# Performance work log

Measured on AMD Instinct MI355X. Metric: run time of the kernel, lower is better.

Reference implementation:

```python
import jax, jax.numpy as jnp
import numpy as np

T, B, H, V = 128, 32, 1024, 32000


def setup_inputs() -> dict:
    key = jax.random.key(0)
    ks = jax.random.split(key, 8)
    scale = 1.0 / np.sqrt(H)
    return {
        "input": jax.random.normal(ks[0], (T, B, H), dtype=jnp.float32),
        "hidden": jnp.zeros((B, H), dtype=jnp.float32),
        "w_ic": jax.random.uniform(ks[1], (H, H), jnp.float32, -scale, scale),
        "w_ix": jax.random.uniform(ks[2], (H, H), jnp.float32, -scale, scale),
        "w_fc": jax.random.uniform(ks[3], (H, H), jnp.float32, -scale, scale),
        "w_fx": jax.random.uniform(ks[4], (H, H), jnp.float32, -scale, scale),
        "b_i": jnp.zeros((H,), dtype=jnp.float32),
        "b_f": jnp.zeros((H,), dtype=jnp.float32),
        "W_out": jax.random.uniform(ks[5], (V, H), jnp.float32, -scale, scale),
        "b_out": jnp.zeros((V,), dtype=jnp.float32),
    }


def reference(input, hidden, w_ic, w_ix, w_fc, w_fx, b_i, b_f, W_out, b_out):
    # Precompute input projections for all timesteps: [T, B, H]
    ix = jnp.einsum("tbh,kh->tbk", input, w_ix)
    fx = jnp.einsum("tbh,kh->tbk", input, w_fx)

    def step(c, xs):
        ix_t, fx_t, x_t = xs
        i_t = jax.nn.sigmoid(c @ w_ic.T + b_i + ix_t)
        f_t = jax.nn.sigmoid(c @ w_fc.T + b_f + fx_t)
        c_new = i_t * x_t + f_t * c  # RAN gated-additive update
        return c_new, c_new

    hidden_final, outputs = jax.lax.scan(step, hidden, (ix, fx, input))
    logits = jnp.einsum("tbh,vh->tbv", outputs, W_out) + b_out
    log_probs = jax.nn.log_softmax(logits, axis=-1)
    return log_probs, hidden_final
```

## Files before the change

kernel.cpp:

```cpp
#include <hip/hip_runtime.h>

typedef __attribute__((ext_vector_type(4))) float f32x4;
typedef __attribute__((ext_vector_type(8))) short bf16x8;

#define T_DIM 128
#define B_DIM 32
#define H_DIM 1024
#define V_DIM 32000
#define MROWS 4096
#define NBLK 64
#define CSTEP 32768
#define WSTRIDE 1028

__device__ __forceinline__ ushort f2bf(float f){
  union { float f; unsigned u; } x; x.f = f;
  unsigned u = x.u;
  unsigned r = (u + 0x7fffu + ((u >> 16) & 1u)) >> 16;
  return (ushort)r;
}
__device__ __forceinline__ float bf2f(ushort h){
  union { unsigned u; float f; } x; x.u = ((unsigned)h) << 16;
  return x.f;
}

__device__ __forceinline__ void async_copy16(void* lds, const void* g){
  __builtin_amdgcn_global_load_lds((const __attribute__((address_space(1))) void*)g,
                                   (__attribute__((address_space(3))) void*)lds, 16, 0, 0);
}

__global__ void cast_bf16_kernel(const float* __restrict__ s, ushort* __restrict__ d, int n4){
  int stride = gridDim.x * blockDim.x;
  for (int i = blockIdx.x*blockDim.x + threadIdx.x; i < n4; i += stride){
    float4 v = ((const float4*)s)[i];
    ushort4 o = make_ushort4(f2bf(v.x), f2bf(v.y), f2bf(v.z), f2bf(v.w));
    ((ushort4*)d)[i] = o;
  }
}

__global__ void cast_split_kernel(const float* __restrict__ s, ushort* __restrict__ dh,
                                  ushort* __restrict__ dl, int n4){
  int stride = gridDim.x * blockDim.x;
  for (int i = blockIdx.x*blockDim.x + threadIdx.x; i < n4; i += stride){
    float4 v = ((const float4*)s)[i];
    ushort4 h = make_ushort4(f2bf(v.x), f2bf(v.y), f2bf(v.z), f2bf(v.w));
    ushort4 l = make_ushort4(f2bf(v.x - bf2f(h.x)), f2bf(v.y - bf2f(h.y)),
                             f2bf(v.z - bf2f(h.z)), f2bf(v.w - bf2f(h.w)));
    ((ushort4*)dh)[i] = h;
    ((ushort4*)dl)[i] = l;
  }
}

__global__ __launch_bounds__(256) void gemm_bt(
    const ushort* __restrict__ A, const ushort* __restrict__ B,
    float* __restrict__ C, const float* __restrict__ bias,
    int N, int K, int NTN, int order, int achunk,
    float* __restrict__ pmax, float* __restrict__ psum)
{
  __shared__ ushort lA[128*32];
  __shared__ ushort lB[128*32];
  __shared__ float pmS[4][64], psS[4][64];
  int tid = threadIdx.x;
  int lane = tid & 63, wid = tid >> 6;
  int bid = blockIdx.x;
  int tm, tn;
  if (order){
    int xcd = bid & 7, id = bid >> 3;
    tn = id >> 2;
    tm = (xcd << 2) | (id & 3);
  } else {
    tm = bid / NTN; tn = bid % NTN;
  }
  int row0 = tm << 7, col0 = tn << 7;

  f32x4 acc[4][4] = {};

  auto stage = [&](const ushort* __restrict__ g, ushort* l, int r0, int k0){
    int c = wid << 1;
    const ushort* s0 = g + (size_t)(r0 + (c<<4) + (lane>>2))*K + k0 + ((lane&3)<<3);
    async_copy16(l + (c<<9), s0);
    async_copy16(l + ((c+1)<<9), s0 + (size_t)16*K);
  };
  auto stageAc = [&](const ushort* __restrict__ g, ushort* l, int r0, int k0){
    int c = wid << 1;
    int cb  = (k0 >> 4) + ((lane & 3) >> 1);
    int sub = (lane & 1) << 3;
    int rA = r0 + (c<<4) + (lane>>2);
    const ushort* sA = g + ((size_t)(rA>>5)<<15) + (cb<<9) + ((rA&31)<<4) + sub;
    async_copy16(l + (c<<9), sA);
    int rB = rA + 16;
    const ushort* sB = g + ((size_t)(rB>>5)<<15) + (cb<<9) + ((rB&31)<<4) + sub;
    async_copy16(l + ((c+1)<<9), sB);
  };

  int nk = K >> 5;
  if (achunk) stageAc(A, lA, row0, 0); else stage(A, lA, row0, 0);
  stage(B, lB, col0, 0);
  int wm = (wid >> 1) << 6, wn = (wid & 1) << 6;
  int kg = (lane >> 4) << 3;
  int ar = lane & 15;

  for (int kt = 0; kt < nk; ++kt){
    __syncthreads();
    bf16x8 af[4], bfr[4];
    #pragma unroll
    for (int mi = 0; mi < 4; ++mi) af[mi]  = *(const bf16x8*)&lA[(wm + mi*16 + ar)*32 + kg];
    #pragma unroll
    for (int ni = 0; ni < 4; ++ni) bfr[ni] = *(const bf16x8*)&lB[(wn + ni*16 + ar)*32 + kg];
    #pragma unroll
    for (int mi = 0; mi < 4; ++mi)
      #pragma unroll
      for (int ni = 0; ni < 4; ++ni)
        acc[mi][ni] = __builtin_amdgcn_mfma_f32_16x16x32_bf16(af[mi], bfr[ni], acc[mi][ni], 0, 0, 0);
    if (kt + 1 < nk){
      __syncthreads();
      if (achunk) stageAc(A, lA, row0, (kt+1) << 5); else stage(A, lA, row0, (kt+1) << 5);
      stage(B, lB, col0, (kt+1) << 5);
    }
  }

  int rr = (lane >> 4) << 2;
  float bb4[4];
  #pragma unroll
  for (int ni = 0; ni < 4; ++ni) bb4[ni] = bias ? bias[col0 + wn + ni*16 + ar] : 0.f;

  #pragma unroll
  for (int mi = 0; mi < 4; ++mi){
    #pragma unroll
    for (int q = 0; q < 4; ++q){
      int r = row0 + wm + mi*16 + rr + q;
      float vals[4];
      #pragma unroll
      for (int ni = 0; ni < 4; ++ni){
        vals[ni] = acc[mi][ni][q] + bb4[ni];
        C[(size_t)r * N + col0 + wn + ni*16 + ar] = vals[ni];
      }
      if (pmax){
        float m = fmaxf(fmaxf(vals[0], vals[1]), fmaxf(vals[2], vals[3]));
        #pragma unroll
        for (int o = 1; o < 16; o <<= 1) m = fmaxf(m, __shfl_xor(m, o));
        float s = expf(vals[0]-m) + expf(vals[1]-m) + expf(vals[2]-m) + expf(vals[3]-m);
        #pragma unroll
        for (int o = 1; o < 16; o <<= 1) s += __shfl_xor(s, o);
        if (ar == 0){ int rl = mi*16 + rr + q; pmS[wid][rl] = m; psS[wid][rl] = s; }
      }
    }
  }
  if (pmax){
    __syncthreads();
    if (tid < 128){
      int rl = tid & 63, half = tid >> 6;
      int w0 = half*2, w1 = w0 + 1;
      float m0 = pmS[w0][rl], m1 = pmS[w1][rl];
      float s0 = psS[w0][rl], s1 = psS[w1][rl];
      float M = fmaxf(m0, m1);
      float S = s0*expf(m0-M) + s1*expf(m1-M);
      int r = row0 + half*64 + rl;
      pmax[(size_t)r*NTN + tn] = M;
      psum[(size_t)r*NTN + tn] = S;
    }
  }
}

__global__ __launch_bounds__(256) void gemm_bt_split(
    const ushort* __restrict__ Ah, const ushort* __restrict__ Al,
    const ushort* __restrict__ Bh, const ushort* __restrict__ Bl,
    float* __restrict__ C, int N, int K, int NTN)
{
  __shared__ ushort lAh[128*32], lAl[128*32], lBh[128*32], lBl[128*32];
  int tid = threadIdx.x;
  int lane = tid & 63, wid = tid >> 6;
  int tm = blockIdx.x / NTN, tn = blockIdx.x % NTN;
  int row0 = tm << 7, col0 = tn << 7;

  f32x4 acc[4][4] = {};

  auto stage = [&](const ushort* __restrict__ g, ushort* l, int r0, int k0){
    int c = wid << 1;
    const ushort* s0 = g + (size_t)(r0 + (c<<4) + (lane>>2))*K + k0 + ((lane&3)<<3);
    async_copy16(l + (c<<9), s0);
    async_copy16(l + ((c+1)<<9), s0 + (size_t)16*K);
  };

  int nk = K >> 5;
  stage(Ah, lAh, row0, 0); stage(Al, lAl, row0, 0);
  stage(Bh, lBh, col0, 0); stage(Bl, lBl, col0, 0);
  int wm = (wid >> 1) << 6, wn = (wid & 1) << 6;
  int kg = (lane >> 4) << 3;
  int ar = lane & 15;

  for (int kt = 0; kt < nk; ++kt){
    __syncthreads();
    bf16x8 afh[4], afl[4], bfh[4], bfl[4];
    #pragma unroll
    for (int mi = 0; mi < 4; ++mi){
      afh[mi] = *(const bf16x8*)&lAh[(wm + mi*16 + ar)*32 + kg];
      afl[mi] = *(const bf16x8*)&lAl[(wm + mi*16 + ar)*32 + kg];
    }
    #pragma unroll
    for (int ni = 0; ni < 4; ++ni){
      bfh[ni] = *(const bf16x8*)&lBh[(wn + ni*16 + ar)*32 + kg];
      bfl[ni] = *(const bf16x8*)&lBl[(wn + ni*16 + ar)*32 + kg];
    }
    #pragma unroll
    for (int mi = 0; mi < 4; ++mi)
      #pragma unroll
      for (int ni = 0; ni < 4; ++ni){
        acc[mi][ni] = __builtin_amdgcn_mfma_f32_16x16x32_bf16(afh[mi], bfh[ni], acc[mi][ni], 0, 0, 0);
        acc[mi][ni] = __builtin_amdgcn_mfma_f32_16x16x32_bf16(afh[mi], bfl[ni], acc[mi][ni], 0, 0, 0);
        acc[mi][ni] = __builtin_amdgcn_mfma_f32_16x16x32_bf16(afl[mi], bfh[ni], acc[mi][ni], 0, 0, 0);
      }
    if (kt + 1 < nk){
      __syncthreads();
      stage(Ah, lAh, row0, (kt+1) << 5); stage(Al, lAl, row0, (kt+1) << 5);
      stage(Bh, lBh, col0, (kt+1) << 5); stage(Bl, lBl, col0, (kt+1) << 5);
    }
  }

  int rr = (lane >> 4) << 2;
  #pragma unroll
  for (int mi = 0; mi < 4; ++mi)
    #pragma unroll
    for (int ni = 0; ni < 4; ++ni){
      int r  = row0 + wm + mi*16 + rr;
      int cc = col0 + wn + ni*16 + ar;
      #pragma unroll
      for (int q = 0; q < 4; ++q)
        C[(size_t)(r + q) * N + cc] = acc[mi][ni][q];
    }
}

__global__ __launch_bounds__(512) void ran_all(
    const ushort* __restrict__ cinit, ushort* __restrict__ cstate,
    const float* __restrict__ hiddenf,
    const ushort* __restrict__ wh, const ushort* __restrict__ wl,
    const float* __restrict__ b_i, const float* __restrict__ b_f,
    const float* __restrict__ ixfx, const float* __restrict__ x_all,
    float* __restrict__ hid_final, unsigned* __restrict__ slots)
{
  __shared__ ushort lWh[32*WSTRIDE];
  __shared__ ushort lWl[32*WSTRIDE];
  __shared__ f32x4 part[4][2][2][64];
  __shared__ float gsm[2*32*17];
  __shared__ float cfl[32][17];

  int tid = threadIdx.x, lane = tid & 63, wid = tid >> 6;
  int kq = wid & 3, mh = wid >> 2;
  int rgate = wid & 1, rmh = wid >> 1;
  int bid = blockIdx.x;
  int nb = bid << 4;
  int ar = lane & 15, kg = (lane >> 4) << 3;
  int um8 = tid >> 3, ukp = (tid & 7) << 1;

  #pragma unroll
  for (int u = 0; u < 8; ++u){
    int unit = u*512 + tid;
    int r = unit >> 7, off = (unit & 127) << 3;
    int g = r >> 4, c = r & 15;
    size_t gsrc = (size_t)((g<<10) + nb + c) * H_DIM + off;
    *(bf16x8*)&lWh[r*WSTRIDE + off] = *(const bf16x8*)&wh[gsrc];
    *(bf16x8*)&lWl[r*WSTRIDE + off] = *(const bf16x8*)&wl[gsrc];
  }
  if (tid < 256){
    cfl[um8][ukp]   = hiddenf[(um8<<10) + nb + ukp];
    cfl[um8][ukp+1] = hiddenf[(um8<<10) + nb + ukp + 1];
  }
  float bb = (rgate ? b_f : b_i)[nb + ar];
  const ushort* b0h = &lWh[(     ar)*WSTRIDE + (kq<<8) + kg];
  const ushort* b0l = &lWl[(     ar)*WSTRIDE + (kq<<8) + kg];
  const ushort* b1h = &lWh[(16 + ar)*WSTRIDE + (kq<<8) + kg];
  const ushort* b1l = &lWl[(16 + ar)*WSTRIDE + (kq<<8) + kg];
  int abase = (kq<<13) + ((kg>>4)<<9) + (((mh<<4) + ar)<<4) + (kg & 8);
  __syncthreads();

  float2 xv2; float pix[4];
  if (tid < 256) xv2 = *(const float2*)&x_all[(um8<<10) + nb + ukp];
  if (wid < 4){
    #pragma unroll
    for (int q = 0; q < 4; ++q){
      int m = (rmh<<4) + ((lane>>4)<<2) + q;
      pix[q] = ixfx[m*2048 + (rgate<<10) + nb + ar];
    }
  }

  for (int t = 0; t < T_DIM; ++t){
    const ushort* cst = t ? cstate + (size_t)(t-1)*CSTEP : cinit;

    bf16x8 a[8];
    #pragma unroll
    for (int kk = 0; kk < 8; ++kk)
      a[kk] = *(const bf16x8*)&cst[abase + (kk<<10)];

    f32x4 g0h = {}, g0l = {}, g1h = {}, g1l = {};
    #pragma unroll
    for (int kk = 0; kk < 8; ++kk){
      int ob = kk << 5;
      bf16x8 w0h = *(const bf16x8*)&b0h[ob];
      bf16x8 w0l = *(const bf16x8*)&b0l[ob];
      bf16x8 w1h = *(const bf16x8*)&b1h[ob];
      bf16x8 w1l = *(const bf16x8*)&b1l[ob];
      g0h = __builtin_amdgcn_mfma_f32_16x16x32_bf16(a[kk], w0h, g0h, 0, 0, 0);
      g0l = __builtin_amdgcn_mfma_f32_16x16x32_bf16(a[kk], w0l, g0l, 0, 0, 0);
      g1h = __builtin_amdgcn_mfma_f32_16x16x32_bf16(a[kk], w1h, g1h, 0, 0, 0);
      g1l = __builtin_amdgcn_mfma_f32_16x16x32_bf16(a[kk], w1l, g1l, 0, 0, 0);
    }
    part[kq][mh][0][lane] = g0h + g0l;
    part[kq][mh][1][lane] = g1h + g1l;
    __syncthreads();

    if (wid < 4){
      f32x4 sum = part[0][rmh][rgate][lane] + part[1][rmh][rgate][lane]
                + part[2][rmh][rgate][lane] + part[3][rmh][rgate][lane];
      #pragma unroll
      for (int q = 0; q < 4; ++q){
        int m = (rmh<<4) + ((lane>>4)<<2) + q;
        float pre = sum[q] + bb + pix[q];
        gsm[((rgate<<5) + m)*17 + ar] = 1.f / (1.f + expf(-pre));
      }
    }
    __syncthreads();

    if (tid < 256){
      float iv0 = gsm[um8*17 + ukp],       iv1 = gsm[um8*17 + ukp + 1];
      float fv0 = gsm[(32+um8)*17 + ukp],  fv1 = gsm[(32+um8)*17 + ukp + 1];
      float c0 = cfl[um8][ukp], c1 = cfl[um8][ukp+1];
      float n0 = iv0*xv2.x + fv0*c0;
      float n1 = iv1*xv2.y + fv1*c1;
      cfl[um8][ukp] = n0; cfl[um8][ukp+1] = n1;
      unsigned hp = (unsigned)f2bf(n0) | ((unsigned)f2bf(n1) << 16);
      size_t cb = (size_t)t*CSTEP + (bid<<9) + (um8<<4) + ukp;
      __hip_atomic_store((unsigned*)&cstate[cb], hp, __ATOMIC_RELAXED, __HIP_MEMORY_SCOPE_AGENT);
      if (t == T_DIM-1){
        int rb = (um8<<10) + nb + ukp;
        hid_final[rb] = n0; hid_final[rb+1] = n1;
      }
    }
    if (t < T_DIM-1){
      __syncthreads();
      if (tid == 0)
        __hip_atomic_store(&slots[bid], (unsigned)(t+1), __ATOMIC_RELAXED, __HIP_MEMORY_SCOPE_AGENT);
      {
        const float* x_t  = x_all + (size_t)(t+1)*(B_DIM*H_DIM);
        const float* ix_t = ixfx  + (size_t)(t+1)*(B_DIM*2048);
        if (tid < 256) xv2 = *(const float2*)&x_t[(um8<<10) + nb + ukp];
        if (wid < 4){
          #pragma unroll
          for (int q = 0; q < 4; ++q){
            int m = (rmh<<4) + ((lane>>4)<<2) + q;
            pix[q] = ix_t[m*2048 + (rgate<<10) + nb + ar];
          }
        }
      }
      if (wid == 7){
        unsigned tgt = (unsigned)(t+1);
        while (1){
          unsigned v = __hip_atomic_load(&slots[lane], __ATOMIC_RELAXED, __HIP_MEMORY_SCOPE_AGENT);
          if (__ballot(v < tgt) == 0ull) break;
          __builtin_amdgcn_s_sleep(1);
        }
      }
      __syncthreads();
    }
  }
}

__global__ void init_c_kernel(const float* __restrict__ hidden,
                              ushort* __restrict__ cinit, unsigned* __restrict__ slots){
  int i = blockIdx.x * blockDim.x + threadIdx.x;
  if (blockIdx.x == 0 && threadIdx.x < NBLK) slots[threadIdx.x] = 0;
  float v = hidden[i];
  int m = i >> 10, col = i & 1023;
  cinit[((col>>4)<<9) + (m<<4) + (col&15)] = f2bf(v);
}

__global__ __launch_bounds__(64) void lse_reduce(const float* __restrict__ pmax,
                                                 const float* __restrict__ psum,
                                                 float* __restrict__ lse, int ntn){
  int row = blockIdx.x, lane = threadIdx.x;
  float m = -1e30f, s = 0.f;
  for (int i = lane; i < ntn; i += 64){
    float mi = pmax[(size_t)row*ntn + i], si = psum[(size_t)row*ntn + i];
    float M = fmaxf(m, mi);
    s = s*expf(m - M) + si*expf(mi - M);
    m = M;
  }
  #pragma unroll
  for (int o = 32; o; o >>= 1){
    float m2 = __shfl_xor(m, o), s2 = __shfl_xor(s, o);
    float M = fmaxf(m, m2);
    s = s*expf(m - M) + s2*expf(m2 - M);
    m = M;
  }
  if (lane == 0) lse[row] = m + logf(s);
}

__global__ __launch_bounds__(256) void sub_kernel(float* __restrict__ logits,
                                                  const float* __restrict__ lse){
  size_t row = blockIdx.x;
  float l = lse[row];
  float4* p4 = (float4*)(logits + row * (size_t)V_DIM);
  for (int i = threadIdx.x; i < V_DIM/4; i += 256){
    float4 v = p4[i];
    v.x -= l; v.y -= l; v.z -= l; v.w -= l;
    p4[i] = v;
  }
}

extern "C" void kernel_launch(void* const* d_in, const int* in_sizes, int n_in,
                              void* d_out, int out_size, void* d_ws, size_t ws_size,
                              hipStream_t stream)
{
  const float* input  = (const float*)d_in[0];
  const float* hidden = (const float*)d_in[1];
  const float* w_ic   = (const float*)d_in[2];
  const float* w_ix   = (const float*)d_in[3];
  const float* w_fc   = (const float*)d_in[4];
  const float* w_fx   = (const float*)d_in[5];
  const float* b_i    = (const float*)d_in[6];
  const float* b_f    = (const float*)d_in[7];
  const float* W_out  = (const float*)d_in[8];
  const float* b_out  = (const float*)d_in[9];
  float* out = (float*)d_out;

  char* ws = (char*)d_ws;
  ushort* wout_bf = (ushort*)(ws + 0);
  ushort* in_hi   = (ushort*)(ws + 65536000);
  ushort* in_lo   = (ushort*)(ws + 73924608);
  ushort* wx_hi   = (ushort*)(ws + 82313216);
  ushort* wx_lo   = (ushort*)(ws + 86507520);
  ushort* wc_hi   = (ushort*)(ws + 90701824);
  ushort* wc_lo   = (ushort*)(ws + 94896128);
  unsigned* slots = (unsigned*)(ws + 107479040);
  ushort* cinit   = (ushort*)(ws + 107479296);
  ushort* cstate  = in_hi;
  float*  pmax    = (float*)in_lo;
  float*  psum    = (float*)(ws + 78020608);
  float*  lse     = (float*)wx_hi;
  float*  ixfx    = out;

  cast_bf16_kernel <<<2048,256,0,stream>>>(W_out, wout_bf, V_DIM*H_DIM/4);
  cast_split_kernel<<<1024,256,0,stream>>>(input, in_hi, in_lo, MROWS*H_DIM/4);
  cast_split_kernel<<<256,256,0,stream>>>(w_ix, wx_hi,             wx_lo,             H_DIM*H_DIM/4);
  cast_split_kernel<<<256,256,0,stream>>>(w_fx, wx_hi+H_DIM*H_DIM, wx_lo+H_DIM*H_DIM, H_DIM*H_DIM/4);
  cast_split_kernel<<<256,256,0,stream>>>(w_ic, wc_hi,             wc_lo,             H_DIM*H_DIM/4);
  cast_split_kernel<<<256,256,0,stream>>>(w_fc, wc_hi+H_DIM*H_DIM, wc_lo+H_DIM*H_DIM, H_DIM*H_DIM/4);

  gemm_bt_split<<<32*16,256,0,stream>>>(in_hi, in_lo, wx_hi, wx_lo, ixfx, 2048, H_DIM, 16);

  init_c_kernel<<<128,256,0,stream>>>(hidden, cinit, slots);

  ran_all<<<NBLK,512,0,stream>>>(cinit, cstate, hidden, wc_hi, wc_lo, b_i, b_f,
                                 ixfx, input, out + (size_t)MROWS*V_DIM, slots);

  gemm_bt<<<32*250,256,0,stream>>>(cstate, wout_bf, out, b_out, V_DIM, H_DIM, 250, 1, 1, pmax, psum);
  lse_reduce<<<MROWS,64,0,stream>>>(pmax, psum, lse, 250);
  sub_kernel<<<MROWS,256,0,stream>>>(out, lse);
}
```

Baseline: 2.037 ms.

## Replace slot-flag grid barrier with per-element tagged state publishing

The recurrent kernel no longer uses a per-block slot counter plus a polling barrier. Each hidden element is now published as a 32-bit word holding the bf16 value and a timestep tag, and consumers poll the data words directly with cache-bypassing loads until every tag matches. This is meant to remove the extra barrier round trip and the separate flag latency on every step. The cost is doubled state traffic, a memset of the tagged buffer, an extra untag kernel before the output GEMM, and a bounded spin that could give up silently after too many retries.

```diff
diff --git a/kernel.cpp b/kernel.cpp
--- a/kernel.cpp
+++ b/kernel.cpp
@@ -2,6 +2,7 @@
 
 typedef __attribute__((ext_vector_type(4))) float f32x4;
 typedef __attribute__((ext_vector_type(8))) short bf16x8;
+typedef __attribute__((ext_vector_type(4))) unsigned u32x4;
 
 #define T_DIM 128
 #define B_DIM 32
@@ -10,6 +11,7 @@
 #define MROWS 4096
 #define NBLK 64
 #define CSTEP 32768
+#define PUBSTEP 32768
 #define WSTRIDE 1028
 
 __device__ __forceinline__ ushort f2bf(float f){
@@ -230,12 +232,11 @@
 }
 
 __global__ __launch_bounds__(512) void ran_all(
-    const ushort* __restrict__ cinit, ushort* __restrict__ cstate,
-    const float* __restrict__ hiddenf,
+    unsigned* __restrict__ pub, const float* __restrict__ hiddenf,
     const ushort* __restrict__ wh, const ushort* __restrict__ wl,
     const float* __restrict__ b_i, const float* __restrict__ b_f,
     const float* __restrict__ ixfx, const float* __restrict__ x_all,
-    float* __restrict__ hid_final, unsigned* __restrict__ slots)
+    float* __restrict__ hid_final)
 {
   __shared__ ushort lWh[32*WSTRIDE];
   __shared__ ushort lWl[32*WSTRIDE];
@@ -245,11 +246,11 @@
 
   int tid = threadIdx.x, lane = tid & 63, wid = tid >> 6;
   int kq = wid & 3, mh = wid >> 2;
-  int rgate = wid & 1, rmh = wid >> 1;
+  int rgate = wid & 1, rmh = (wid >> 1) & 1;
   int bid = blockIdx.x;
   int nb = bid << 4;
   int ar = lane & 15, kg = (lane >> 4) << 3;
-  int um8 = tid >> 3, ukp = (tid & 7) << 1;
+  int um = tid >> 4, uk = tid & 15;
 
   #pragma unroll
   for (int u = 0; u < 8; ++u){
@@ -260,10 +261,7 @@
     *(bf16x8*)&lWh[r*WSTRIDE + off] = *(const bf16x8*)&wh[gsrc];
     *(bf16x8*)&lWl[r*WSTRIDE + off] = *(const bf16x8*)&wl[gsrc];
   }
-  if (tid < 256){
-    cfl[um8][ukp]   = hiddenf[(um8<<10) + nb + ukp];
-    cfl[um8][ukp+1] = hiddenf[(um8<<10) + nb + ukp + 1];
-  }
+  cfl[um][uk] = hiddenf[(um<<10) + nb + uk];
   float bb = (rgate ? b_f : b_i)[nb + ar];
   const ushort* b0h = &lWh[(     ar)*WSTRIDE + (kq<<8) + kg];
   const ushort* b0l = &lWl[(     ar)*WSTRIDE + (kq<<8) + kg];
@@ -272,36 +270,59 @@
   int abase = (kq<<13) + ((kg>>4)<<9) + (((mh<<4) + ar)<<4) + (kg & 8);
   __syncthreads();
 
-  float2 xv2; float pix[4];
-  if (tid < 256) xv2 = *(const float2*)&x_all[(um8<<10) + nb + ukp];
-  if (wid < 4){
-    #pragma unroll
-    for (int q = 0; q < 4; ++q){
-      int m = (rmh<<4) + ((lane>>4)<<2) + q;
-      pix[q] = ixfx[m*2048 + (rgate<<10) + nb + ar];
-    }
-  }
-
   for (int t = 0; t < T_DIM; ++t){
-    const ushort* cst = t ? cstate + (size_t)(t-1)*CSTEP : cinit;
-
-    bf16x8 a[8];
-    #pragma unroll
-    for (int kk = 0; kk < 8; ++kk)
-      a[kk] = *(const bf16x8*)&cst[abase + (kk<<10)];
+    float xq1 = x_all[((size_t)t<<15) + (um<<10) + nb + uk];
+    float pix[4];
+    if (wid < 4){
+      const float* ix_t = ixfx + ((size_t)t<<16);
+      #pragma unroll
+      for (int q = 0; q < 4; ++q){
+        int m = (rmh<<4) + ((lane>>4)<<2) + q;
+        pix[q] = ix_t[m*2048 + (rgate<<10) + nb + ar];
+      }
+    }
+
+    const unsigned* ps = pub + ((size_t)t << 15) + abase;
+    unsigned expt = (unsigned)(t + 1) << 16;
+    u32x4 w0[8], w1[8];
+    int tries = 0;
+    while (1){
+      #pragma unroll
+      for (int f = 0; f < 8; ++f){
+        const unsigned* p = ps + (f << 10);
+        asm volatile("global_load_dwordx4 %0, %2, off sc0 sc1\n\t"
+                     "global_load_dwordx4 %1, %2, off offset:16 sc0 sc1"
+                     : "=&v"(w0[f]), "=&v"(w1[f]) : "v"(p));
+      }
+      asm volatile("s_waitcnt vmcnt(0)" ::: "memory");
+      __builtin_amdgcn_sched_barrier(0);
+      unsigned bad = 0;
+      #pragma unroll
+      for (int f = 0; f < 8; ++f){
+        bad |= (w0[f][0]^expt)|(w0[f][1]^expt)|(w0[f][2]^expt)|(w0[f][3]^expt)
+             | (w1[f][0]^expt)|(w1[f][1]^expt)|(w1[f][2]^expt)|(w1[f][3]^expt);
+      }
+      if (__ballot((bad & 0xFFFF0000u) != 0) == 0ull) break;
+      if (++tries > (1<<15)) break;
+    }
 
     f32x4 g0h = {}, g0l = {}, g1h = {}, g1l = {};
     #pragma unroll
-    for (int kk = 0; kk < 8; ++kk){
-      int ob = kk << 5;
-      bf16x8 w0h = *(const bf16x8*)&b0h[ob];
-      bf16x8 w0l = *(const bf16x8*)&b0l[ob];
-      bf16x8 w1h = *(const bf16x8*)&b1h[ob];
-      bf16x8 w1l = *(const bf16x8*)&b1l[ob];
-      g0h = __builtin_amdgcn_mfma_f32_16x16x32_bf16(a[kk], w0h, g0h, 0, 0, 0);
-      g0l = __builtin_amdgcn_mfma_f32_16x16x32_bf16(a[kk], w0l, g0l, 0, 0, 0);
-      g1h = __builtin_amdgcn_mfma_f32_16x16x32_bf16(a[kk], w1h, g1h, 0, 0, 0);
-      g1l = __builtin_amdgcn_mfma_f32_16x16x32_bf16(a[kk], w1l, g1l, 0, 0, 0);
+    for (int f = 0; f < 8; ++f){
+      union { unsigned u[4]; bf16x8 v; } cv;
+      cv.u[0] = (w0[f][0] & 0xFFFFu) | (w0[f][1] << 16);
+      cv.u[1] = (w0[f][2] & 0xFFFFu) | (w0[f][3] << 16);
+      cv.u[2] = (w1[f][0] & 0xFFFFu) | (w1[f][1] << 16);
+      cv.u[3] = (w1[f][2] & 0xFFFFu) | (w1[f][3] << 16);
+      int ob = f << 5;
+      bf16x8 v0h = *(const bf16x8*)&b0h[ob];
+      bf16x8 v0l = *(const bf16x8*)&b0l[ob];
+      bf16x8 v1h = *(const bf16x8*)&b1h[ob];
+      bf16x8 v1l = *(const bf16x8*)&b1l[ob];
+      g0h = __builtin_amdgcn_mfma_f32_16x16x32_bf16(cv.v, v0h, g0h, 0, 0, 0);
+      g0l = __builtin_amdgcn_mfma_f32_16x16x32_bf16(cv.v, v0l, g0l, 0, 0, 0);
+      g1h = __builtin_amdgcn_mfma_f32_16x16x32_bf16(cv.v, v1h, g1h, 0, 0, 0);
+      g1l = __builtin_amdgcn_mfma_f32_16x16x32_bf16(cv.v, v1l, g1l, 0, 0, 0);
     }
     part[kq][mh][0][lane] = g0h + g0l;
     part[kq][mh][1][lane] = g1h + g1l;
@@ -319,57 +340,34 @@
     }
     __syncthreads();
 
-    if (tid < 256){
-      float iv0 = gsm[um8*17 + ukp],       iv1 = gsm[um8*17 + ukp + 1];
-      float fv0 = gsm[(32+um8)*17 + ukp],  fv1 = gsm[(32+um8)*17 + ukp + 1];
-      float c0 = cfl[um8][ukp], c1 = cfl[um8][ukp+1];
-      float n0 = iv0*xv2.x + fv0*c0;
-      float n1 = iv1*xv2.y + fv1*c1;
-      cfl[um8][ukp] = n0; cfl[um8][ukp+1] = n1;
-      unsigned hp = (unsigned)f2bf(n0) | ((unsigned)f2bf(n1) << 16);
-      size_t cb = (size_t)t*CSTEP + (bid<<9) + (um8<<4) + ukp;
-      __hip_atomic_store((unsigned*)&cstate[cb], hp, __ATOMIC_RELAXED, __HIP_MEMORY_SCOPE_AGENT);
-      if (t == T_DIM-1){
-        int rb = (um8<<10) + nb + ukp;
-        hid_final[rb] = n0; hid_final[rb+1] = n1;
-      }
-    }
-    if (t < T_DIM-1){
-      __syncthreads();
-      if (tid == 0)
-        __hip_atomic_store(&slots[bid], (unsigned)(t+1), __ATOMIC_RELAXED, __HIP_MEMORY_SCOPE_AGENT);
-      {
-        const float* x_t  = x_all + (size_t)(t+1)*(B_DIM*H_DIM);
-        const float* ix_t = ixfx  + (size_t)(t+1)*(B_DIM*2048);
-        if (tid < 256) xv2 = *(const float2*)&x_t[(um8<<10) + nb + ukp];
-        if (wid < 4){
-          #pragma unroll
-          for (int q = 0; q < 4; ++q){
-            int m = (rmh<<4) + ((lane>>4)<<2) + q;
-            pix[q] = ix_t[m*2048 + (rgate<<10) + nb + ar];
-          }
-        }
-      }
-      if (wid == 7){
-        unsigned tgt = (unsigned)(t+1);
-        while (1){
-          unsigned v = __hip_atomic_load(&slots[lane], __ATOMIC_RELAXED, __HIP_MEMORY_SCOPE_AGENT);
-          if (__ballot(v < tgt) == 0ull) break;
-          __builtin_amdgcn_s_sleep(1);
-        }
-      }
-      __syncthreads();
-    }
-  }
-}
-
-__global__ void init_c_kernel(const float* __restrict__ hidden,
-                              ushort* __restrict__ cinit, unsigned* __restrict__ slots){
+    {
+      float iv = gsm[um*17 + uk];
+      float fv = gsm[(32+um)*17 + uk];
+      float cv2 = cfl[um][uk];
+      float cn = iv * xq1 + fv * cv2;
+      cfl[um][uk] = cn;
+      unsigned word = ((unsigned)(t + 2) << 16) | (unsigned)f2bf(cn);
+      __hip_atomic_store(&pub[((size_t)(t+1) << 15) + (bid << 9) + tid], word,
+                         __ATOMIC_RELAXED, __HIP_MEMORY_SCOPE_AGENT);
+      if (t == T_DIM-1) hid_final[(um<<10) + nb + uk] = cn;
+    }
+    __syncthreads();
+  }
+}
+
+__global__ void init_c_kernel(const float* __restrict__ hidden, unsigned* __restrict__ pub){
   int i = blockIdx.x * blockDim.x + threadIdx.x;
-  if (blockIdx.x == 0 && threadIdx.x < NBLK) slots[threadIdx.x] = 0;
   float v = hidden[i];
   int m = i >> 10, col = i & 1023;
-  cinit[((col>>4)<<9) + (m<<4) + (col&15)] = f2bf(v);
+  pub[((col>>4)<<9) + (m<<4) + (col&15)] = (1u << 16) | (unsigned)f2bf(v);
+}
+
+__global__ void untag_kernel(const unsigned* __restrict__ pub, ushort* __restrict__ cst){
+  int e = (blockIdx.x * blockDim.x + threadIdx.x) << 2;
+  int s = e >> 15, w = e & 32767;
+  const unsigned* p = pub + ((size_t)(s + 1) << 15) + w;
+  ushort4 o = make_ushort4((ushort)p[0], (ushort)p[1], (ushort)p[2], (ushort)p[3]);
+  *(ushort4*)&cst[e] = o;
 }
 
 __global__ __launch_bounds__(64) void lse_reduce(const float* __restrict__ pmax,
@@ -429,12 +427,11 @@
   ushort* wx_lo   = (ushort*)(ws + 86507520);
   ushort* wc_hi   = (ushort*)(ws + 90701824);
   ushort* wc_lo   = (ushort*)(ws + 94896128);
-  unsigned* slots = (unsigned*)(ws + 107479040);
-  ushort* cinit   = (ushort*)(ws + 107479296);
-  ushort* cstate  = in_hi;
-  float*  pmax    = (float*)in_lo;
-  float*  psum    = (float*)(ws + 78020608);
-  float*  lse     = (float*)wx_hi;
+  unsigned* pub   = (unsigned*)(ws + 65536000);
+  ushort* cstate  = (ushort*)(ws + 82444288);
+  float*  pmax    = (float*)(ws + 94896128);
+  float*  psum    = (float*)(ws + 99090432);
+  float*  lse     = (float*)(ws + 103186432);
   float*  ixfx    = out;
 
   cast_bf16_kernel <<<2048,256,0,stream>>>(W_out, wout_bf, V_DIM*H_DIM/4);
@@ -446,11 +443,13 @@
 
   gemm_bt_split<<<32*16,256,0,stream>>>(in_hi, in_lo, wx_hi, wx_lo, ixfx, 2048, H_DIM, 16);
 
-  init_c_kernel<<<128,256,0,stream>>>(hidden, cinit, slots);
-
-  ran_all<<<NBLK,512,0,stream>>>(cinit, cstate, hidden, wc_hi, wc_lo, b_i, b_f,
-                                 ixfx, input, out + (size_t)MROWS*V_DIM, slots);
-
+  hipMemsetAsync(pub, 0, (size_t)129 * PUBSTEP * 4, stream);
+  init_c_kernel<<<128,256,0,stream>>>(hidden, pub);
+
+  ran_all<<<NBLK,512,0,stream>>>(pub, hidden, wc_hi, wc_lo, b_i, b_f,
+                                 ixfx, input, out + (size_t)MROWS*V_DIM);
+
+  untag_kernel<<<4096,256,0,stream>>>(pub, cstate);
   gemm_bt<<<32*250,256,0,stream>>>(cstate, wout_bf, out, b_out, V_DIM, H_DIM, 250, 1, 1, pmax, psum);
   lse_reduce<<<MROWS,64,0,stream>>>(pmax, psum, lse, 250);
   sub_kernel<<<MROWS,256,0,stream>>>(out, lse);
```

New measurement: 1.999 ms. About the same (-1.9%).
